# Optimization experiments

Measured on AMD Instinct MI355X. Metric: run time of the kernel, lower is better.

Reference implementation:

```python
import jax, jax.numpy as jnp
import numpy as np

N_HEADS = 12
C = 3          # per-head in/hidden/out channels (12/4)
C_PRED = 1     # predictor hidden (4/4)
BN_EPS = 1e-5
COS_EPS = 1e-8
B, H, W = 8, 512, 768


def setup_inputs() -> dict:
    key = jax.random.key(0)
    ks = jax.random.split(key, 22)
    p = lambda k, s: jax.random.normal(k, s, jnp.float32) * 0.1
    return {
        "latent1": jax.random.normal(ks[0], (B, N_HEADS, H, W), jnp.float32),
        "latent2": jax.random.normal(ks[1], (B, N_HEADS, H, W), jnp.float32),
        # projector conv1 + BN
        "W1": p(ks[2], (N_HEADS, C, C)), "b1": p(ks[3], (N_HEADS, C)),
        "g1": 1.0 + p(ks[4], (N_HEADS, C)), "be1": p(ks[5], (N_HEADS, C)),
        # projector conv2 + BN
        "W2": p(ks[6], (N_HEADS, C, C)), "b2": p(ks[7], (N_HEADS, C)),
        "g2": 1.0 + p(ks[8], (N_HEADS, C)), "be2": p(ks[9], (N_HEADS, C)),
        # projector conv3 + BN (no ReLU)
        "W3": p(ks[10], (N_HEADS, C, C)), "b3": p(ks[11], (N_HEADS, C)),
        "g3": 1.0 + p(ks[12], (N_HEADS, C)), "be3": p(ks[13], (N_HEADS, C)),
        # predictor conv1 + BN
        "W4": p(ks[14], (N_HEADS, C_PRED, C)), "b4": p(ks[15], (N_HEADS, C_PRED)),
        "g4": 1.0 + p(ks[16], (N_HEADS, C_PRED)), "be4": p(ks[17], (N_HEADS, C_PRED)),
        # predictor conv2 (no BN)
        "W5": p(ks[18], (N_HEADS, C, C_PRED)), "b5": p(ks[19], (N_HEADS, C)),
    }


def _conv1x1(x, Wk, bk):
    # x: [B, Cin, H, W'], Wk: [Cout, Cin]
    return jnp.einsum('oc,bchw->bohw', Wk, x) + bk[None, :, None, None]


def _bn(x, g, be):
    # training-mode BatchNorm2d: batch statistics over (B, H, W)
    m = x.mean(axis=(0, 2, 3), keepdims=True)
    v = x.var(axis=(0, 2, 3), keepdims=True)  # biased var, as torch BN uses
    return (x - m) * jax.lax.rsqrt(v + BN_EPS) * g[None, :, None, None] + be[None, :, None, None]


def _cos_loss(p, z):
    # -mean(cosine_similarity(p, detach(z), dim=1))
    z = jax.lax.stop_gradient(z)
    dot = jnp.sum(p * z, axis=1)
    npn = jnp.maximum(jnp.sqrt(jnp.sum(p * p, axis=1)), COS_EPS)
    nzn = jnp.maximum(jnp.sqrt(jnp.sum(z * z, axis=1)), COS_EPS)
    return -jnp.mean(dot / (npn * nzn))


def _head_loss(x1, x2, W1, b1, g1, be1, W2, b2, g2, be2, W3, b3, g3, be3,
               W4, b4, g4, be4, W5, b5):
    def proj(x):
        x = jax.nn.relu(_bn(_conv1x1(x, W1, b1), g1, be1))
        x = jax.nn.relu(_bn(_conv1x1(x, W2, b2), g2, be2))
        return _bn(_conv1x1(x, W3, b3), g3, be3)

    def pred(z):
        h = jax.nn.relu(_bn(_conv1x1(z, W4, b4), g4, be4))
        return _conv1x1(h, W5, b5)

    z1, z2 = proj(x1), proj(x2)
    p1, p2 = pred(z1), pred(z2)
    return 0.5 * (_cos_loss(p1, z2) + _cos_loss(p2, z1))


def reference(latent1, latent2, W1, b1, g1, be1, W2, b2, g2, be2,
              W3, b3, g3, be3, W4, b4, g4, be4, W5, b5):
    Bd, Cd, Hd, Wd = latent1.shape
    Wp = Wd // C
    # per-channel view [B, H, W] -> [B, 3, H, W/3]; stack heads on leading axis
    x1 = latent1.reshape(Bd, N_HEADS, C, Hd, Wp).transpose(1, 0, 2, 3, 4)
    x2 = latent2.reshape(Bd, N_HEADS, C, Hd, Wp).transpose(1, 0, 2, 3, 4)
    losses = jax.vmap(_head_loss)(x1, x2, W1, b1, g1, be1, W2, b2, g2, be2,
                                  W3, b3, g3, be3, W4, b4, g4, be4, W5, b5)
    return jnp.sum(losses)
```

## Files before the change

kernel.cpp:

```cpp
#include <hip/hip_runtime.h>
#include <hip/hip_fp16.h>
#include <math.h>


typedef unsigned short ushort_t;
typedef unsigned int   uint_t;

constexpr int   NH      = 12;
constexpr int   POS     = 131072;
constexpr int   NB      = 8;
constexpr long long MLL = (long long)NB * POS;
constexpr int   CSPAN   = POS / 16;
constexpr int   SBLK    = 128;
constexpr int   NTOT    = NB * NH * 3 * POS;

constexpr size_t P_CNT      = (size_t)24 * SBLK * 9;
constexpr size_t NEED_BYTES = (size_t)NTOT * 2 * 2 + 3 * P_CNT * 8 + 64;

template <int K>
__device__ inline void block_reduce_to0(double (&v)[K]) {
#pragma unroll
  for (int off = 32; off > 0; off >>= 1) {
#pragma unroll
    for (int k = 0; k < K; ++k) v[k] += __shfl_down(v[k], off, 64);
  }
  __shared__ double lds[4][K];
  __syncthreads();
  const int lane = threadIdx.x & 63;
  const int wv   = threadIdx.x >> 6;
  if (lane == 0) {
#pragma unroll
    for (int k = 0; k < K; ++k) lds[wv][k] = v[k];
  }
  __syncthreads();
  if (threadIdx.x == 0) {
#pragma unroll
    for (int k = 0; k < K; ++k) v[k] = lds[0][k] + lds[1][k] + lds[2][k] + lds[3][k];
  }
}

__device__ inline uint_t pack2h(float lo, float hi) {
  return (uint_t)__half_as_ushort(__float2half(lo)) |
         ((uint_t)__half_as_ushort(__float2half(hi)) << 16);
}
__device__ inline float h_lo(uint_t w) {
  return __half2float(__ushort_as_half((unsigned short)(w & 0xFFFFu)));
}
__device__ inline float h_hi(uint_t w) {
  return __half2float(__ushort_as_half((unsigned short)(w >> 16)));
}

template <bool H16>
__device__ inline void load3x8(const float* __restrict__ X,
                               const ushort_t* __restrict__ XH,
                               size_t e, float (&f)[3][8]) {
#pragma unroll
  for (int c = 0; c < 3; ++c) {
    const size_t a = e + (size_t)c * POS;
    if constexpr (H16) {
      const uint4 v = *(const uint4*)(XH + a);
      f[c][0] = h_lo(v.x); f[c][1] = h_hi(v.x);
      f[c][2] = h_lo(v.y); f[c][3] = h_hi(v.y);
      f[c][4] = h_lo(v.z); f[c][5] = h_hi(v.z);
      f[c][6] = h_lo(v.w); f[c][7] = h_hi(v.w);
    } else {
      const float4 u0 = *(const float4*)(X + a);
      const float4 u1 = *(const float4*)(X + a + 4);
      f[c][0] = u0.x; f[c][1] = u0.y; f[c][2] = u0.z; f[c][3] = u0.w;
      f[c][4] = u1.x; f[c][5] = u1.y; f[c][6] = u1.z; f[c][7] = u1.w;
    }
  }
}

__device__ inline void store8h(ushort_t* __restrict__ XH, size_t e,
                               const float (&g)[8]) {
  uint4 h;
  h.x = pack2h(g[0], g[1]);
  h.y = pack2h(g[2], g[3]);
  h.z = pack2h(g[4], g[5]);
  h.w = pack2h(g[6], g[7]);
  *(uint4*)(XH + e) = h;
}

__device__ inline void moments_to_mc(const double (&v)[9], double (&m)[3],
                                     double (&C)[3][3]) {
  const double M = (double)MLL;
  m[0] = v[0] / M; m[1] = v[1] / M; m[2] = v[2] / M;
  C[0][0] = v[3] / M - m[0] * m[0];
  C[1][1] = v[4] / M - m[1] * m[1];
  C[2][2] = v[5] / M - m[2] * m[2];
  C[0][1] = C[1][0] = v[6] / M - m[0] * m[1];
  C[0][2] = C[2][0] = v[7] / M - m[0] * m[2];
  C[1][2] = C[2][1] = v[8] / M - m[1] * m[2];
}

__device__ inline void slice_reduce9(const double* __restrict__ P, int s,
                                     double (&v)[9]) {
#pragma unroll
  for (int k = 0; k < 9; ++k) v[k] = 0.0;
  if (threadIdx.x < SBLK) {
    const double* p = P + ((size_t)s * SBLK + threadIdx.x) * 9;
#pragma unroll
    for (int k = 0; k < 9; ++k) v[k] = p[k];
  }
  block_reduce_to0<9>(v);
}

__device__ inline void fold_math(const double (&v)[9], const float* __restrict__ Wk,
                                 const float* __restrict__ bk,
                                 const float* __restrict__ gk,
                                 const float* __restrict__ bek, int n,
                                 float* __restrict__ dst) {
  double m[3], C[3][3];
  moments_to_mc(v, m, C);
  for (int o = 0; o < 3; ++o) {
    const double w0 = Wk[n * 9 + o * 3 + 0];
    const double w1 = Wk[n * 9 + o * 3 + 1];
    const double w2 = Wk[n * 9 + o * 3 + 2];
    const double my = w0 * m[0] + w1 * m[1] + w2 * m[2] + (double)bk[n * 3 + o];
    const double vy = w0 * w0 * C[0][0] + w1 * w1 * C[1][1] + w2 * w2 * C[2][2] +
                      2.0 * (w0 * w1 * C[0][1] + w0 * w2 * C[0][2] + w1 * w2 * C[1][2]);
    const double sc = (double)gk[n * 3 + o] / sqrt(vy + 1e-5);
    const double tt = (double)bek[n * 3 + o] - my * sc;
    dst[o * 3 + 0] = (float)(sc * w0);
    dst[o * 3 + 1] = (float)(sc * w1);
    dst[o * 3 + 2] = (float)(sc * w2);
    dst[9 + o]     = (float)(sc * (double)bk[n * 3 + o] + tt);
  }
}

__device__ inline void fold34_math(const double (&v)[9], const float* __restrict__ W3,
                                   const float* __restrict__ b3,
                                   const float* __restrict__ g3,
                                   const float* __restrict__ be3,
                                   const float* __restrict__ W4,
                                   const float* __restrict__ b4,
                                   const float* __restrict__ g4,
                                   const float* __restrict__ be4, int n,
                                   float* __restrict__ dst) {
  double m[3], C[3][3];
  moments_to_mc(v, m, C);
  double F3d[3][3], c3d[3];
  for (int o = 0; o < 3; ++o) {
    const double w0 = W3[n * 9 + o * 3 + 0];
    const double w1 = W3[n * 9 + o * 3 + 1];
    const double w2 = W3[n * 9 + o * 3 + 2];
    const double m3 = w0 * m[0] + w1 * m[1] + w2 * m[2] + (double)b3[n * 3 + o];
    const double vy = w0 * w0 * C[0][0] + w1 * w1 * C[1][1] + w2 * w2 * C[2][2] +
                      2.0 * (w0 * w1 * C[0][1] + w0 * w2 * C[0][2] + w1 * w2 * C[1][2]);
    const double s3 = (double)g3[n * 3 + o] / sqrt(vy + 1e-5);
    const double t3 = (double)be3[n * 3 + o] - m3 * s3;
    F3d[o][0] = s3 * w0; F3d[o][1] = s3 * w1; F3d[o][2] = s3 * w2;
    c3d[o] = s3 * (double)b3[n * 3 + o] + t3;
    dst[o * 3 + 0] = (float)F3d[o][0];
    dst[o * 3 + 1] = (float)F3d[o][1];
    dst[o * 3 + 2] = (float)F3d[o][2];
    dst[9 + o]     = (float)c3d[o];
  }
  double q[3] = {0.0, 0.0, 0.0};
  double d = (double)b4[n];
  for (int o = 0; o < 3; ++o) {
    const double w4o = W4[n * 3 + o];
    q[0] += w4o * F3d[o][0];
    q[1] += w4o * F3d[o][1];
    q[2] += w4o * F3d[o][2];
    d += w4o * c3d[o];
  }
  const double m4 = q[0] * m[0] + q[1] * m[1] + q[2] * m[2] + d;
  double v4 = 0.0;
  for (int i = 0; i < 3; ++i)
    for (int j = 0; j < 3; ++j) v4 += q[i] * q[j] * C[i][j];
  const double s4 = (double)g4[n] / sqrt(v4 + 1e-5);
  const double t4 = (double)be4[n] - m4 * s4;
  for (int o = 0; o < 3; ++o) dst[12 + o] = (float)(s4 * (double)W4[n * 3 + o]);
  dst[15] = (float)(s4 * (double)b4[n] + t4);
}

template <bool STORE>
__global__ __launch_bounds__(256) void pass1_kernel(
    const float* __restrict__ x1, const float* __restrict__ x2,
    ushort_t* __restrict__ xh1, ushort_t* __restrict__ xh2,
    double* __restrict__ P0, double* __restrict__ lossAcc,
    uint_t* __restrict__ cnt) {
  if (blockIdx.x == 0 && blockIdx.y == 0 && threadIdx.x == 0) {
    *lossAcc = 0.0;
    *cnt = 0u;
  }
  const int u = blockIdx.y;
  const int s = u % 24;
  const int b = u / 24;
  const int n = s >> 1;
  const float* __restrict__ X = (s & 1) ? x2 : x1;
  ushort_t* __restrict__ XH = (s & 1) ? xh2 : xh1;
  const size_t off0 = (size_t)((b * NH + n) * 3) * POS + (size_t)blockIdx.x * CSPAN;

  float acc[9] = {0.f, 0.f, 0.f, 0.f, 0.f, 0.f, 0.f, 0.f, 0.f};
#pragma unroll 2
  for (int i = 0; i < 4; ++i) {
    const size_t e = off0 + i * 2048 + threadIdx.x * 8;
    float f[3][8];
    load3x8<false>(X, nullptr, e, f);
    if constexpr (STORE) {
#pragma unroll
      for (int c = 0; c < 3; ++c) store8h(XH, e + (size_t)c * POS, f[c]);
    }
#pragma unroll
    for (int j = 0; j < 8; ++j) {
      const float X0 = f[0][j], X1 = f[1][j], X2 = f[2][j];
      acc[0] += X0;      acc[1] += X1;      acc[2] += X2;
      acc[3] += X0 * X0; acc[4] += X1 * X1; acc[5] += X2 * X2;
      acc[6] += X0 * X1; acc[7] += X0 * X2; acc[8] += X1 * X2;
    }
  }
  double v9[9];
#pragma unroll
  for (int k = 0; k < 9; ++k) v9[k] = (double)acc[k];
  block_reduce_to0<9>(v9);
  if (threadIdx.x == 0) {
    double* dst = P0 + ((size_t)s * SBLK + b * 16 + blockIdx.x) * 9;
#pragma unroll
    for (int k = 0; k < 9; ++k) dst[k] = v9[k];
  }
}

template <bool H16>
__global__ __launch_bounds__(256) void pass2_kernel(
    const float* __restrict__ x1, const float* __restrict__ x2,
    const ushort_t* __restrict__ xh1, const ushort_t* __restrict__ xh2,
    const float* __restrict__ W1, const float* __restrict__ b1,
    const float* __restrict__ g1, const float* __restrict__ be1,
    const double* __restrict__ P0, double* __restrict__ P1) {
  const int u = blockIdx.y;
  const int s = u % 24;
  const int b = u / 24;
  const int n = s >> 1;
  const float* __restrict__ X = (s & 1) ? x2 : x1;
  const ushort_t* __restrict__ XH = (s & 1) ? xh2 : xh1;
  const size_t off0 = (size_t)((b * NH + n) * 3) * POS + (size_t)blockIdx.x * CSPAN;

  __shared__ float sf1[12];
  {
    double v[9];
    slice_reduce9(P0, s, v);
    if (threadIdx.x == 0) fold_math(v, W1, b1, g1, be1, n, sf1);
    __syncthreads();
  }
  float w1f[3][3], c1v[3];
#pragma unroll
  for (int o = 0; o < 3; ++o) {
#pragma unroll
    for (int c = 0; c < 3; ++c) w1f[o][c] = sf1[o * 3 + c];
    c1v[o] = sf1[9 + o];
  }

  float acc[9] = {0.f, 0.f, 0.f, 0.f, 0.f, 0.f, 0.f, 0.f, 0.f};
#pragma unroll 2
  for (int i = 0; i < 4; ++i) {
    const size_t e = off0 + i * 2048 + threadIdx.x * 8;
    float f[3][8];
    load3x8<H16>(X, XH, e, f);
#pragma unroll
    for (int j = 0; j < 8; ++j) {
      const float X0 = f[0][j], X1 = f[1][j], X2 = f[2][j];
      const float A0 = fmaxf(0.f, fmaf(w1f[0][0], X0, fmaf(w1f[0][1], X1, fmaf(w1f[0][2], X2, c1v[0]))));
      const float A1 = fmaxf(0.f, fmaf(w1f[1][0], X0, fmaf(w1f[1][1], X1, fmaf(w1f[1][2], X2, c1v[1]))));
      const float A2v= fmaxf(0.f, fmaf(w1f[2][0], X0, fmaf(w1f[2][1], X1, fmaf(w1f[2][2], X2, c1v[2]))));
      acc[0] += A0;       acc[1] += A1;       acc[2] += A2v;
      acc[3] += A0 * A0;  acc[4] += A1 * A1;  acc[5] += A2v * A2v;
      acc[6] += A0 * A1;  acc[7] += A0 * A2v; acc[8] += A1 * A2v;
    }
  }
  double v9[9];
#pragma unroll
  for (int k = 0; k < 9; ++k) v9[k] = (double)acc[k];
  block_reduce_to0<9>(v9);
  if (threadIdx.x == 0) {
    double* dst = P1 + ((size_t)s * SBLK + b * 16 + blockIdx.x) * 9;
#pragma unroll
    for (int k = 0; k < 9; ++k) dst[k] = v9[k];
  }
}

template <bool H16>
__global__ __launch_bounds__(256) void pass3_kernel(
    const float* __restrict__ x1, const float* __restrict__ x2,
    const ushort_t* __restrict__ xh1, const ushort_t* __restrict__ xh2,
    const float* __restrict__ W1, const float* __restrict__ b1,
    const float* __restrict__ g1, const float* __restrict__ be1,
    const float* __restrict__ W2, const float* __restrict__ b2,
    const float* __restrict__ g2, const float* __restrict__ be2,
    const double* __restrict__ P0, const double* __restrict__ P1,
    double* __restrict__ P2) {
  const int u = blockIdx.y;
  const int s = u % 24;
  const int b = u / 24;
  const int n = s >> 1;
  const float* __restrict__ X = (s & 1) ? x2 : x1;
  const ushort_t* __restrict__ XH = (s & 1) ? xh2 : xh1;
  const size_t off0 = (size_t)((b * NH + n) * 3) * POS + (size_t)blockIdx.x * CSPAN;

  __shared__ float sf1[12], sf2[12];
  {
    double v[9];
    slice_reduce9(P0, s, v);
    if (threadIdx.x == 0) fold_math(v, W1, b1, g1, be1, n, sf1);
    slice_reduce9(P1, s, v);
    if (threadIdx.x == 0) fold_math(v, W2, b2, g2, be2, n, sf2);
    __syncthreads();
  }
  float w1f[3][3], c1v[3], w2f[3][3], c2v[3];
#pragma unroll
  for (int o = 0; o < 3; ++o) {
#pragma unroll
    for (int c = 0; c < 3; ++c) {
      w1f[o][c] = sf1[o * 3 + c];
      w2f[o][c] = sf2[o * 3 + c];
    }
    c1v[o] = sf1[9 + o];
    c2v[o] = sf2[9 + o];
  }

  float acc[9] = {0.f, 0.f, 0.f, 0.f, 0.f, 0.f, 0.f, 0.f, 0.f};
#pragma unroll 2
  for (int i = 0; i < 4; ++i) {
    const size_t e = off0 + i * 2048 + threadIdx.x * 8;
    float f[3][8];
    load3x8<H16>(X, XH, e, f);
#pragma unroll
    for (int j = 0; j < 8; ++j) {
      const float X0 = f[0][j], X1 = f[1][j], X2 = f[2][j];
      const float a0 = fmaxf(0.f, fmaf(w1f[0][0], X0, fmaf(w1f[0][1], X1, fmaf(w1f[0][2], X2, c1v[0]))));
      const float a1 = fmaxf(0.f, fmaf(w1f[1][0], X0, fmaf(w1f[1][1], X1, fmaf(w1f[1][2], X2, c1v[1]))));
      const float a2 = fmaxf(0.f, fmaf(w1f[2][0], X0, fmaf(w1f[2][1], X1, fmaf(w1f[2][2], X2, c1v[2]))));
      const float A0 = fmaxf(0.f, fmaf(w2f[0][0], a0, fmaf(w2f[0][1], a1, fmaf(w2f[0][2], a2, c2v[0]))));
      const float A1 = fmaxf(0.f, fmaf(w2f[1][0], a0, fmaf(w2f[1][1], a1, fmaf(w2f[1][2], a2, c2v[1]))));
      const float A2v= fmaxf(0.f, fmaf(w2f[2][0], a0, fmaf(w2f[2][1], a1, fmaf(w2f[2][2], a2, c2v[2]))));
      acc[0] += A0;       acc[1] += A1;       acc[2] += A2v;
      acc[3] += A0 * A0;  acc[4] += A1 * A1;  acc[5] += A2v * A2v;
      acc[6] += A0 * A1;  acc[7] += A0 * A2v; acc[8] += A1 * A2v;
    }
  }
  double v9[9];
#pragma unroll
  for (int k = 0; k < 9; ++k) v9[k] = (double)acc[k];
  block_reduce_to0<9>(v9);
  if (threadIdx.x == 0) {
    double* dst = P2 + ((size_t)s * SBLK + b * 16 + blockIdx.x) * 9;
#pragma unroll
    for (int k = 0; k < 9; ++k) dst[k] = v9[k];
  }
}

__device__ inline void full_chain(const float (&S)[40], const float (&w5)[3],
                                  const float (&b5v)[3], float v0, float v1,
                                  float v2, float (&z)[3], float (&p)[3]) {
  const float t0 = fmaxf(0.f, fmaf(S[0], v0, fmaf(S[1], v1, fmaf(S[2], v2, S[9]))));
  const float t1 = fmaxf(0.f, fmaf(S[3], v0, fmaf(S[4], v1, fmaf(S[5], v2, S[10]))));
  const float t2 = fmaxf(0.f, fmaf(S[6], v0, fmaf(S[7], v1, fmaf(S[8], v2, S[11]))));
  const float a0 = fmaxf(0.f, fmaf(S[12], t0, fmaf(S[13], t1, fmaf(S[14], t2, S[21]))));
  const float a1 = fmaxf(0.f, fmaf(S[15], t0, fmaf(S[16], t1, fmaf(S[17], t2, S[22]))));
  const float a2 = fmaxf(0.f, fmaf(S[18], t0, fmaf(S[19], t1, fmaf(S[20], t2, S[23]))));
  z[0] = fmaf(S[24], a0, fmaf(S[25], a1, fmaf(S[26], a2, S[33])));
  z[1] = fmaf(S[27], a0, fmaf(S[28], a1, fmaf(S[29], a2, S[34])));
  z[2] = fmaf(S[30], a0, fmaf(S[31], a1, fmaf(S[32], a2, S[35])));
  const float y4 = fmaf(S[36], z[0], fmaf(S[37], z[1], fmaf(S[38], z[2], S[39])));
  const float h = fmaxf(0.f, y4);
#pragma unroll
  for (int o = 0; o < 3; ++o) p[o] = fmaf(w5[o], h, b5v[o]);
}

template <bool H16>
__global__ __launch_bounds__(256) void pass4_kernel(
    const float* __restrict__ x1, const float* __restrict__ x2,
    const ushort_t* __restrict__ xh1, const ushort_t* __restrict__ xh2,
    const float* __restrict__ W1, const float* __restrict__ b1,
    const float* __restrict__ g1, const float* __restrict__ be1,
    const float* __restrict__ W2, const float* __restrict__ b2,
    const float* __restrict__ g2, const float* __restrict__ be2,
    const float* __restrict__ W3, const float* __restrict__ b3,
    const float* __restrict__ g3, const float* __restrict__ be3,
    const float* __restrict__ W4, const float* __restrict__ b4,
    const float* __restrict__ g4, const float* __restrict__ be4,
    const float* __restrict__ W5, const float* __restrict__ b5,
    const double* __restrict__ P0, const double* __restrict__ P1,
    const double* __restrict__ P2, double* __restrict__ lossAcc,
    uint_t* __restrict__ cnt, float* __restrict__ out) {
  const int u = blockIdx.y;
  const int n = u % 12;
  const int b = u / 12;
  const size_t off0 = (size_t)((b * NH + n) * 3) * POS + (size_t)blockIdx.x * CSPAN;

  __shared__ float sh[2][40];
  {
    double v[9];
#pragma unroll
    for (int br = 0; br < 2; ++br) {
      const int s = 2 * n + br;
      slice_reduce9(P0, s, v);
      if (threadIdx.x == 0) fold_math(v, W1, b1, g1, be1, n, &sh[br][0]);
      slice_reduce9(P1, s, v);
      if (threadIdx.x == 0) fold_math(v, W2, b2, g2, be2, n, &sh[br][12]);
      slice_reduce9(P2, s, v);
      if (threadIdx.x == 0)
        fold34_math(v, W3, b3, g3, be3, W4, b4, g4, be4, n, &sh[br][24]);
    }
    __syncthreads();
  }
  float S0[40], S1[40];
#pragma unroll
  for (int k = 0; k < 40; ++k) {
    S0[k] = sh[0][k];
    S1[k] = sh[1][k];
  }
  float w5[3], b5v[3];
#pragma unroll
  for (int o = 0; o < 3; ++o) {
    w5[o]  = W5[n * 3 + o];
    b5v[o] = b5[n * 3 + o];
  }

  float acc = 0.f;
  for (int i = 0; i < 4; ++i) {
    const size_t e = off0 + i * 2048 + threadIdx.x * 8;
    float fA[3][8], fB[3][8];
    load3x8<H16>(x1, xh1, e, fA);
    load3x8<H16>(x2, xh2, e, fB);
#pragma unroll
    for (int j = 0; j < 8; ++j) {
      float z1[3], p1[3], z2[3], p2[3];
      full_chain(S0, w5, b5v, fA[0][j], fA[1][j], fA[2][j], z1, p1);
      full_chain(S1, w5, b5v, fB[0][j], fB[1][j], fB[2][j], z2, p2);

      const float d12 = p1[0] * z2[0] + p1[1] * z2[1] + p1[2] * z2[2];
      const float pp1 = p1[0] * p1[0] + p1[1] * p1[1] + p1[2] * p1[2];
      const float zz2 = z2[0] * z2[0] + z2[1] * z2[1] + z2[2] * z2[2];
      acc += d12 * __builtin_amdgcn_rsqf(fmaxf(pp1, 1e-16f)) *
                   __builtin_amdgcn_rsqf(fmaxf(zz2, 1e-16f));

      const float d21 = p2[0] * z1[0] + p2[1] * z1[1] + p2[2] * z1[2];
      const float pp2 = p2[0] * p2[0] + p2[1] * p2[1] + p2[2] * p2[2];
      const float zz1 = z1[0] * z1[0] + z1[1] * z1[1] + z1[2] * z1[2];
      acc += d21 * __builtin_amdgcn_rsqf(fmaxf(pp2, 1e-16f)) *
                   __builtin_amdgcn_rsqf(fmaxf(zz1, 1e-16f));
    }
  }

  double v[1] = {(double)acc};
  block_reduce_to0<1>(v);
  if (threadIdx.x == 0) {
    atomicAdd(lossAcc, v[0]);
    __threadfence();
    const uint_t total = gridDim.x * gridDim.y;
    const uint_t old = atomicAdd(cnt, 1u);
    if (old == total - 1u) {
      __threadfence();
      const double tot = atomicAdd(lossAcc, 0.0);
      out[0] = (float)(-0.5 * tot / (double)MLL);
    }
  }
}

extern "C" void kernel_launch(void* const* d_in, const int* in_sizes, int n_in,
                              void* d_out, int out_size, void* d_ws, size_t ws_size,
                              hipStream_t stream) {
  const float* x1  = (const float*)d_in[0];
  const float* x2  = (const float*)d_in[1];
  const float* W1  = (const float*)d_in[2];
  const float* b1  = (const float*)d_in[3];
  const float* g1  = (const float*)d_in[4];
  const float* be1 = (const float*)d_in[5];
  const float* W2  = (const float*)d_in[6];
  const float* b2  = (const float*)d_in[7];
  const float* g2  = (const float*)d_in[8];
  const float* be2 = (const float*)d_in[9];
  const float* W3  = (const float*)d_in[10];
  const float* b3  = (const float*)d_in[11];
  const float* g3  = (const float*)d_in[12];
  const float* be3 = (const float*)d_in[13];
  const float* W4  = (const float*)d_in[14];
  const float* b4  = (const float*)d_in[15];
  const float* g4  = (const float*)d_in[16];
  const float* be4 = (const float*)d_in[17];
  const float* W5  = (const float*)d_in[18];
  const float* b5  = (const float*)d_in[19];

  const bool big = ws_size >= NEED_BYTES;
  ushort_t* xh1 = nullptr;
  ushort_t* xh2 = nullptr;
  double* dbase;
  if (big) {
    xh1 = (ushort_t*)d_ws;
    xh2 = xh1 + NTOT;
    dbase = (double*)(xh2 + NTOT);
  } else {
    dbase = (double*)d_ws;
  }
  double* P0 = dbase;
  double* P1 = P0 + P_CNT;
  double* P2 = P1 + P_CNT;
  double* lossAcc = P2 + P_CNT;
  uint_t* cnt = (uint_t*)(lossAcc + 1);

  const dim3 blk(256);
  const dim3 gA(16, 192);
  const dim3 gD(16, 96);

  if (big) {
    pass1_kernel<true><<<gA, blk, 0, stream>>>(x1, x2, xh1, xh2, P0, lossAcc, cnt);
    pass2_kernel<true><<<gA, blk, 0, stream>>>(x1, x2, xh1, xh2, W1, b1, g1, be1,
                                               P0, P1);
    pass3_kernel<true><<<gA, blk, 0, stream>>>(x1, x2, xh1, xh2, W1, b1, g1, be1,
                                               W2, b2, g2, be2, P0, P1, P2);
    pass4_kernel<true><<<gD, blk, 0, stream>>>(x1, x2, xh1, xh2, W1, b1, g1, be1,
                                               W2, b2, g2, be2, W3, b3, g3, be3,
                                               W4, b4, g4, be4, W5, b5, P0, P1,
                                               P2, lossAcc, cnt, (float*)d_out);
  } else {
    pass1_kernel<false><<<gA, blk, 0, stream>>>(x1, x2, nullptr, nullptr, P0,
                                                lossAcc, cnt);
    pass2_kernel<false><<<gA, blk, 0, stream>>>(x1, x2, nullptr, nullptr, W1, b1,
                                                g1, be1, P0, P1);
    pass3_kernel<false><<<gA, blk, 0, stream>>>(x1, x2, nullptr, nullptr, W1, b1,
                                                g1, be1, W2, b2, g2, be2, P0, P1,
                                                P2);
    pass4_kernel<false><<<gD, blk, 0, stream>>>(x1, x2, nullptr, nullptr, W1, b1,
                                                g1, be1, W2, b2, g2, be2, W3, b3,
                                                g3, be3, W4, b4, g4, be4, W5, b5,
                                                P0, P1, P2, lossAcc, cnt,
                                                (float*)d_out);
  }
}
```

Before: 580.4 us.

## Hoist BN stat folding into tiny kernels and software-prefetch pass loads

Before, every block of passes 2-4 re-reduced all per-slice partial moments and recomputed the folded BN affine parameters in its prologue. That work now runs once per slice in small stats/fold kernels that write a derived-parameter buffer, and the big passes just read it. The pass loops also explicitly double-buffer the next iteration's vector loads to overlap memory latency with compute. The cost is three extra kernel launches and higher register pressure from the prefetch buffers.

```diff
diff --git a/kernel.cpp b/kernel.cpp
--- a/kernel.cpp
+++ b/kernel.cpp
@@ -15,7 +15,8 @@
 constexpr int   NTOT    = NB * NH * 3 * POS;
 
 constexpr size_t P_CNT      = (size_t)24 * SBLK * 9;
-constexpr size_t NEED_BYTES = (size_t)NTOT * 2 * 2 + 3 * P_CNT * 8 + 64;
+constexpr size_t NEED_BYTES = (size_t)NTOT * 2 * 2 + 3 * P_CNT * 8 + 32 +
+                              (size_t)24 * 40 * 4;
 
 template <int K>
 __device__ inline void block_reduce_to0(double (&v)[K]) {
@@ -43,33 +44,11 @@
   return (uint_t)__half_as_ushort(__float2half(lo)) |
          ((uint_t)__half_as_ushort(__float2half(hi)) << 16);
 }
-__device__ inline float h_lo(uint_t w) {
-  return __half2float(__ushort_as_half((unsigned short)(w & 0xFFFFu)));
-}
-__device__ inline float h_hi(uint_t w) {
-  return __half2float(__ushort_as_half((unsigned short)(w >> 16)));
-}
-
-template <bool H16>
-__device__ inline void load3x8(const float* __restrict__ X,
-                               const ushort_t* __restrict__ XH,
-                               size_t e, float (&f)[3][8]) {
-#pragma unroll
-  for (int c = 0; c < 3; ++c) {
-    const size_t a = e + (size_t)c * POS;
-    if constexpr (H16) {
-      const uint4 v = *(const uint4*)(XH + a);
-      f[c][0] = h_lo(v.x); f[c][1] = h_hi(v.x);
-      f[c][2] = h_lo(v.y); f[c][3] = h_hi(v.y);
-      f[c][4] = h_lo(v.z); f[c][5] = h_hi(v.z);
-      f[c][6] = h_lo(v.w); f[c][7] = h_hi(v.w);
-    } else {
-      const float4 u0 = *(const float4*)(X + a);
-      const float4 u1 = *(const float4*)(X + a + 4);
-      f[c][0] = u0.x; f[c][1] = u0.y; f[c][2] = u0.z; f[c][3] = u0.w;
-      f[c][4] = u1.x; f[c][5] = u1.y; f[c][6] = u1.z; f[c][7] = u1.w;
-    }
-  }
+
+__device__ inline float hget(const uint4& v, int j) {
+  const uint_t w = (&v.x)[j >> 1];
+  return __half2float(__ushort_as_half(
+      (j & 1) ? (unsigned short)(w >> 16) : (unsigned short)(w & 0xFFFFu)));
 }
 
 __device__ inline void store8h(ushort_t* __restrict__ XH, size_t e,
@@ -92,18 +71,6 @@
   C[0][1] = C[1][0] = v[6] / M - m[0] * m[1];
   C[0][2] = C[2][0] = v[7] / M - m[0] * m[2];
   C[1][2] = C[2][1] = v[8] / M - m[1] * m[2];
-}
-
-__device__ inline void slice_reduce9(const double* __restrict__ P, int s,
-                                     double (&v)[9]) {
-#pragma unroll
-  for (int k = 0; k < 9; ++k) v[k] = 0.0;
-  if (threadIdx.x < SBLK) {
-    const double* p = P + ((size_t)s * SBLK + threadIdx.x) * 9;
-#pragma unroll
-    for (int k = 0; k < 9; ++k) v[k] = p[k];
-  }
-  block_reduce_to0<9>(v);
 }
 
 __device__ inline void fold_math(const double (&v)[9], const float* __restrict__ Wk,
@@ -176,6 +143,24 @@
   dst[15] = (float)(s4 * (double)b4[n] + t4);
 }
 
+__device__ inline void acc9(float X0, float X1, float X2, float (&a)[9]) {
+  a[0] += X0;      a[1] += X1;      a[2] += X2;
+  a[3] += X0 * X0; a[4] += X1 * X1; a[5] += X2 * X2;
+  a[6] += X0 * X1; a[7] += X0 * X2; a[8] += X1 * X2;
+}
+
+__device__ inline void load3x8_f32(const float* __restrict__ X, size_t e,
+                                   float (&f)[3][8]) {
+#pragma unroll
+  for (int c = 0; c < 3; ++c) {
+    const size_t a = e + (size_t)c * POS;
+    const float4 u0 = *(const float4*)(X + a);
+    const float4 u1 = *(const float4*)(X + a + 4);
+    f[c][0] = u0.x; f[c][1] = u0.y; f[c][2] = u0.z; f[c][3] = u0.w;
+    f[c][4] = u1.x; f[c][5] = u1.y; f[c][6] = u1.z; f[c][7] = u1.w;
+  }
+}
+
 template <bool STORE>
 __global__ __launch_bounds__(256) void pass1_kernel(
     const float* __restrict__ x1, const float* __restrict__ x2,
@@ -192,26 +177,50 @@
   const int n = s >> 1;
   const float* __restrict__ X = (s & 1) ? x2 : x1;
   ushort_t* __restrict__ XH = (s & 1) ? xh2 : xh1;
+  const int tid = threadIdx.x;
   const size_t off0 = (size_t)((b * NH + n) * 3) * POS + (size_t)blockIdx.x * CSPAN;
 
   float acc[9] = {0.f, 0.f, 0.f, 0.f, 0.f, 0.f, 0.f, 0.f, 0.f};
-#pragma unroll 2
+
+  float4 cur[6];
+#pragma unroll
+  for (int c = 0; c < 3; ++c) {
+    const size_t a = off0 + (size_t)c * POS + tid * 8;
+    cur[2 * c]     = *(const float4*)(X + a);
+    cur[2 * c + 1] = *(const float4*)(X + a + 4);
+  }
+#pragma unroll
   for (int i = 0; i < 4; ++i) {
-    const size_t e = off0 + i * 2048 + threadIdx.x * 8;
+    float4 nxt[6];
+    if (i < 3) {
+#pragma unroll
+      for (int c = 0; c < 3; ++c) {
+        const size_t a = off0 + (size_t)c * POS + (i + 1) * 2048 + tid * 8;
+        nxt[2 * c]     = *(const float4*)(X + a);
+        nxt[2 * c + 1] = *(const float4*)(X + a + 4);
+      }
+    }
+    const size_t e = off0 + i * 2048 + tid * 8;
     float f[3][8];
-    load3x8<false>(X, nullptr, e, f);
+#pragma unroll
+    for (int c = 0; c < 3; ++c) {
+      f[c][0] = cur[2 * c].x;     f[c][1] = cur[2 * c].y;
+      f[c][2] = cur[2 * c].z;     f[c][3] = cur[2 * c].w;
+      f[c][4] = cur[2 * c + 1].x; f[c][5] = cur[2 * c + 1].y;
+      f[c][6] = cur[2 * c + 1].z; f[c][7] = cur[2 * c + 1].w;
+    }
     if constexpr (STORE) {
 #pragma unroll
       for (int c = 0; c < 3; ++c) store8h(XH, e + (size_t)c * POS, f[c]);
     }
 #pragma unroll
-    for (int j = 0; j < 8; ++j) {
-      const float X0 = f[0][j], X1 = f[1][j], X2 = f[2][j];
-      acc[0] += X0;      acc[1] += X1;      acc[2] += X2;
-      acc[3] += X0 * X0; acc[4] += X1 * X1; acc[5] += X2 * X2;
-      acc[6] += X0 * X1; acc[7] += X0 * X2; acc[8] += X1 * X2;
-    }
-  }
+    for (int j = 0; j < 8; ++j) acc9(f[0][j], f[1][j], f[2][j], acc);
+    if (i < 3) {
+#pragma unroll
+      for (int k = 0; k < 6; ++k) cur[k] = nxt[k];
+    }
+  }
+
   double v9[9];
 #pragma unroll
   for (int k = 0; k < 9; ++k) v9[k] = (double)acc[k];
@@ -223,53 +232,109 @@
   }
 }
 
+__global__ __launch_bounds__(256) void stats_fold_kernel(
+    const double* __restrict__ P, const float* __restrict__ Wk,
+    const float* __restrict__ bk, const float* __restrict__ gk,
+    const float* __restrict__ bek, float* __restrict__ derived, int outoff) {
+  const int s = blockIdx.x;
+  double v[9] = {0, 0, 0, 0, 0, 0, 0, 0, 0};
+  if (threadIdx.x < SBLK) {
+    const double* p = P + ((size_t)s * SBLK + threadIdx.x) * 9;
+#pragma unroll
+    for (int k = 0; k < 9; ++k) v[k] = p[k];
+  }
+  block_reduce_to0<9>(v);
+  if (threadIdx.x == 0)
+    fold_math(v, Wk, bk, gk, bek, s >> 1, derived + s * 40 + outoff);
+}
+
+__global__ __launch_bounds__(256) void stats34_kernel(
+    const double* __restrict__ P2, const float* __restrict__ W3,
+    const float* __restrict__ b3, const float* __restrict__ g3,
+    const float* __restrict__ be3, const float* __restrict__ W4,
+    const float* __restrict__ b4, const float* __restrict__ g4,
+    const float* __restrict__ be4, float* __restrict__ derived) {
+  const int s = blockIdx.x;
+  double v[9] = {0, 0, 0, 0, 0, 0, 0, 0, 0};
+  if (threadIdx.x < SBLK) {
+    const double* p = P2 + ((size_t)s * SBLK + threadIdx.x) * 9;
+#pragma unroll
+    for (int k = 0; k < 9; ++k) v[k] = p[k];
+  }
+  block_reduce_to0<9>(v);
+  if (threadIdx.x == 0)
+    fold34_math(v, W3, b3, g3, be3, W4, b4, g4, be4, s >> 1,
+                derived + s * 40 + 24);
+}
+
 template <bool H16>
 __global__ __launch_bounds__(256) void pass2_kernel(
     const float* __restrict__ x1, const float* __restrict__ x2,
     const ushort_t* __restrict__ xh1, const ushort_t* __restrict__ xh2,
-    const float* __restrict__ W1, const float* __restrict__ b1,
-    const float* __restrict__ g1, const float* __restrict__ be1,
-    const double* __restrict__ P0, double* __restrict__ P1) {
+    const float* __restrict__ derived, double* __restrict__ P1) {
   const int u = blockIdx.y;
   const int s = u % 24;
   const int b = u / 24;
   const int n = s >> 1;
   const float* __restrict__ X = (s & 1) ? x2 : x1;
   const ushort_t* __restrict__ XH = (s & 1) ? xh2 : xh1;
+  const int tid = threadIdx.x;
   const size_t off0 = (size_t)((b * NH + n) * 3) * POS + (size_t)blockIdx.x * CSPAN;
 
-  __shared__ float sf1[12];
-  {
-    double v[9];
-    slice_reduce9(P0, s, v);
-    if (threadIdx.x == 0) fold_math(v, W1, b1, g1, be1, n, sf1);
-    __syncthreads();
-  }
+  const float* D = derived + s * 40;
   float w1f[3][3], c1v[3];
 #pragma unroll
   for (int o = 0; o < 3; ++o) {
 #pragma unroll
-    for (int c = 0; c < 3; ++c) w1f[o][c] = sf1[o * 3 + c];
-    c1v[o] = sf1[9 + o];
+    for (int c = 0; c < 3; ++c) w1f[o][c] = D[o * 3 + c];
+    c1v[o] = D[9 + o];
   }
 
   float acc[9] = {0.f, 0.f, 0.f, 0.f, 0.f, 0.f, 0.f, 0.f, 0.f};
-#pragma unroll 2
-  for (int i = 0; i < 4; ++i) {
-    const size_t e = off0 + i * 2048 + threadIdx.x * 8;
-    float f[3][8];
-    load3x8<H16>(X, XH, e, f);
-#pragma unroll
-    for (int j = 0; j < 8; ++j) {
-      const float X0 = f[0][j], X1 = f[1][j], X2 = f[2][j];
-      const float A0 = fmaxf(0.f, fmaf(w1f[0][0], X0, fmaf(w1f[0][1], X1, fmaf(w1f[0][2], X2, c1v[0]))));
-      const float A1 = fmaxf(0.f, fmaf(w1f[1][0], X0, fmaf(w1f[1][1], X1, fmaf(w1f[1][2], X2, c1v[1]))));
-      const float A2v= fmaxf(0.f, fmaf(w1f[2][0], X0, fmaf(w1f[2][1], X1, fmaf(w1f[2][2], X2, c1v[2]))));
-      acc[0] += A0;       acc[1] += A1;       acc[2] += A2v;
-      acc[3] += A0 * A0;  acc[4] += A1 * A1;  acc[5] += A2v * A2v;
-      acc[6] += A0 * A1;  acc[7] += A0 * A2v; acc[8] += A1 * A2v;
-    }
-  }
+
+  if constexpr (H16) {
+    uint4 cur[3];
+#pragma unroll
+    for (int c = 0; c < 3; ++c)
+      cur[c] = *(const uint4*)(XH + off0 + (size_t)c * POS + tid * 8);
+#pragma unroll
+    for (int i = 0; i < 4; ++i) {
+      uint4 nxt[3];
+      if (i < 3) {
+#pragma unroll
+        for (int c = 0; c < 3; ++c)
+          nxt[c] = *(const uint4*)(XH + off0 + (size_t)c * POS + (i + 1) * 2048 +
+                                   tid * 8);
+      }
+#pragma unroll
+      for (int j = 0; j < 8; ++j) {
+        const float X0 = hget(cur[0], j), X1 = hget(cur[1], j), X2 = hget(cur[2], j);
+        const float A0 = fmaxf(0.f, fmaf(w1f[0][0], X0, fmaf(w1f[0][1], X1, fmaf(w1f[0][2], X2, c1v[0]))));
+        const float A1 = fmaxf(0.f, fmaf(w1f[1][0], X0, fmaf(w1f[1][1], X1, fmaf(w1f[1][2], X2, c1v[1]))));
+        const float A2 = fmaxf(0.f, fmaf(w1f[2][0], X0, fmaf(w1f[2][1], X1, fmaf(w1f[2][2], X2, c1v[2]))));
+        acc9(A0, A1, A2, acc);
+      }
+      if (i < 3) {
+#pragma unroll
+        for (int c = 0; c < 3; ++c) cur[c] = nxt[c];
+      }
+    }
+  } else {
+    for (int i = 0; i < 4; ++i) {
+      const size_t e = off0 + i * 2048 + tid * 8;
+      float f[3][8];
+      load3x8_f32(X, e, f);
+#pragma unroll
+      for (int j = 0; j < 8; ++j) {
+        const float X0 = f[0][j], X1 = f[1][j], X2 = f[2][j];
+        const float A0 = fmaxf(0.f, fmaf(w1f[0][0], X0, fmaf(w1f[0][1], X1, fmaf(w1f[0][2], X2, c1v[0]))));
+        const float A1 = fmaxf(0.f, fmaf(w1f[1][0], X0, fmaf(w1f[1][1], X1, fmaf(w1f[1][2], X2, c1v[1]))));
+        const float A2 = fmaxf(0.f, fmaf(w1f[2][0], X0, fmaf(w1f[2][1], X1, fmaf(w1f[2][2], X2, c1v[2]))));
+        acc9(A0, A1, A2, acc);
+      }
+    }
+  }
+
   double v9[9];
 #pragma unroll
   for (int k = 0; k < 9; ++k) v9[k] = (double)acc[k];
@@ -285,61 +350,73 @@
 __global__ __launch_bounds__(256) void pass3_kernel(
     const float* __restrict__ x1, const float* __restrict__ x2,
     const ushort_t* __restrict__ xh1, const ushort_t* __restrict__ xh2,
-    const float* __restrict__ W1, const float* __restrict__ b1,
-    const float* __restrict__ g1, const float* __restrict__ be1,
-    const float* __restrict__ W2, const float* __restrict__ b2,
-    const float* __restrict__ g2, const float* __restrict__ be2,
-    const double* __restrict__ P0, const double* __restrict__ P1,
-    double* __restrict__ P2) {
+    const float* __restrict__ derived, double* __restrict__ P2) {
   const int u = blockIdx.y;
   const int s = u % 24;
   const int b = u / 24;
   const int n = s >> 1;
   const float* __restrict__ X = (s & 1) ? x2 : x1;
   const ushort_t* __restrict__ XH = (s & 1) ? xh2 : xh1;
+  const int tid = threadIdx.x;
   const size_t off0 = (size_t)((b * NH + n) * 3) * POS + (size_t)blockIdx.x * CSPAN;
 
-  __shared__ float sf1[12], sf2[12];
-  {
-    double v[9];
-    slice_reduce9(P0, s, v);
-    if (threadIdx.x == 0) fold_math(v, W1, b1, g1, be1, n, sf1);
-    slice_reduce9(P1, s, v);
-    if (threadIdx.x == 0) fold_math(v, W2, b2, g2, be2, n, sf2);
-    __syncthreads();
-  }
+  const float* D = derived + s * 40;
   float w1f[3][3], c1v[3], w2f[3][3], c2v[3];
 #pragma unroll
   for (int o = 0; o < 3; ++o) {
 #pragma unroll
     for (int c = 0; c < 3; ++c) {
-      w1f[o][c] = sf1[o * 3 + c];
-      w2f[o][c] = sf2[o * 3 + c];
-    }
-    c1v[o] = sf1[9 + o];
-    c2v[o] = sf2[9 + o];
+      w1f[o][c] = D[o * 3 + c];
+      w2f[o][c] = D[12 + o * 3 + c];
+    }
+    c1v[o] = D[9 + o];
+    c2v[o] = D[21 + o];
   }
 
   float acc[9] = {0.f, 0.f, 0.f, 0.f, 0.f, 0.f, 0.f, 0.f, 0.f};
-#pragma unroll 2
-  for (int i = 0; i < 4; ++i) {
-    const size_t e = off0 + i * 2048 + threadIdx.x * 8;
-    float f[3][8];
-    load3x8<H16>(X, XH, e, f);
-#pragma unroll
-    for (int j = 0; j < 8; ++j) {
-      const float X0 = f[0][j], X1 = f[1][j], X2 = f[2][j];
-      const float a0 = fmaxf(0.f, fmaf(w1f[0][0], X0, fmaf(w1f[0][1], X1, fmaf(w1f[0][2], X2, c1v[0]))));
-      const float a1 = fmaxf(0.f, fmaf(w1f[1][0], X0, fmaf(w1f[1][1], X1, fmaf(w1f[1][2], X2, c1v[1]))));
-      const float a2 = fmaxf(0.f, fmaf(w1f[2][0], X0, fmaf(w1f[2][1], X1, fmaf(w1f[2][2], X2, c1v[2]))));
-      const float A0 = fmaxf(0.f, fmaf(w2f[0][0], a0, fmaf(w2f[0][1], a1, fmaf(w2f[0][2], a2, c2v[0]))));
-      const float A1 = fmaxf(0.f, fmaf(w2f[1][0], a0, fmaf(w2f[1][1], a1, fmaf(w2f[1][2], a2, c2v[1]))));
-      const float A2v= fmaxf(0.f, fmaf(w2f[2][0], a0, fmaf(w2f[2][1], a1, fmaf(w2f[2][2], a2, c2v[2]))));
-      acc[0] += A0;       acc[1] += A1;       acc[2] += A2v;
-      acc[3] += A0 * A0;  acc[4] += A1 * A1;  acc[5] += A2v * A2v;
-      acc[6] += A0 * A1;  acc[7] += A0 * A2v; acc[8] += A1 * A2v;
-    }
-  }
+
+  auto body = [&](float X0, float X1, float X2) {
+    const float a0 = fmaxf(0.f, fmaf(w1f[0][0], X0, fmaf(w1f[0][1], X1, fmaf(w1f[0][2], X2, c1v[0]))));
+    const float a1 = fmaxf(0.f, fmaf(w1f[1][0], X0, fmaf(w1f[1][1], X1, fmaf(w1f[1][2], X2, c1v[1]))));
+    const float a2 = fmaxf(0.f, fmaf(w1f[2][0], X0, fmaf(w1f[2][1], X1, fmaf(w1f[2][2], X2, c1v[2]))));
+    const float A0 = fmaxf(0.f, fmaf(w2f[0][0], a0, fmaf(w2f[0][1], a1, fmaf(w2f[0][2], a2, c2v[0]))));
+    const float A1 = fmaxf(0.f, fmaf(w2f[1][0], a0, fmaf(w2f[1][1], a1, fmaf(w2f[1][2], a2, c2v[1]))));
+    const float A2 = fmaxf(0.f, fmaf(w2f[2][0], a0, fmaf(w2f[2][1], a1, fmaf(w2f[2][2], a2, c2v[2]))));
+    acc9(A0, A1, A2, acc);
+  };
+
+  if constexpr (H16) {
+    uint4 cur[3];
+#pragma unroll
+    for (int c = 0; c < 3; ++c)
+      cur[c] = *(const uint4*)(XH + off0 + (size_t)c * POS + tid * 8);
+#pragma unroll
+    for (int i = 0; i < 4; ++i) {
+      uint4 nxt[3];
+      if (i < 3) {
+#pragma unroll
+        for (int c = 0; c < 3; ++c)
+          nxt[c] = *(const uint4*)(XH + off0 + (size_t)c * POS + (i + 1) * 2048 +
+                                   tid * 8);
+      }
+#pragma unroll
+      for (int j = 0; j < 8; ++j)
+        body(hget(cur[0], j), hget(cur[1], j), hget(cur[2], j));
+      if (i < 3) {
+#pragma unroll
+        for (int c = 0; c < 3; ++c) cur[c] = nxt[c];
+      }
+    }
+  } else {
+    for (int i = 0; i < 4; ++i) {
+      const size_t e = off0 + i * 2048 + tid * 8;
+      float f[3][8];
+      load3x8_f32(X, e, f);
+#pragma unroll
+      for (int j = 0; j < 8; ++j) body(f[0][j], f[1][j], f[2][j]);
+    }
+  }
+
   double v9[9];
 #pragma unroll
   for (int k = 0; k < 9; ++k) v9[k] = (double)acc[k];
@@ -373,44 +450,24 @@
 __global__ __launch_bounds__(256) void pass4_kernel(
     const float* __restrict__ x1, const float* __restrict__ x2,
     const ushort_t* __restrict__ xh1, const ushort_t* __restrict__ xh2,
-    const float* __restrict__ W1, const float* __restrict__ b1,
-    const float* __restrict__ g1, const float* __restrict__ be1,
-    const float* __restrict__ W2, const float* __restrict__ b2,
-    const float* __restrict__ g2, const float* __restrict__ be2,
-    const float* __restrict__ W3, const float* __restrict__ b3,
-    const float* __restrict__ g3, const float* __restrict__ be3,
-    const float* __restrict__ W4, const float* __restrict__ b4,
-    const float* __restrict__ g4, const float* __restrict__ be4,
     const float* __restrict__ W5, const float* __restrict__ b5,
-    const double* __restrict__ P0, const double* __restrict__ P1,
-    const double* __restrict__ P2, double* __restrict__ lossAcc,
+    const float* __restrict__ derived, double* __restrict__ lossAcc,
     uint_t* __restrict__ cnt, float* __restrict__ out) {
   const int u = blockIdx.y;
   const int n = u % 12;
   const int b = u / 12;
+  const int tid = threadIdx.x;
   const size_t off0 = (size_t)((b * NH + n) * 3) * POS + (size_t)blockIdx.x * CSPAN;
 
-  __shared__ float sh[2][40];
+  float S0[40], S1[40];
   {
-    double v[9];
-#pragma unroll
-    for (int br = 0; br < 2; ++br) {
-      const int s = 2 * n + br;
-      slice_reduce9(P0, s, v);
-      if (threadIdx.x == 0) fold_math(v, W1, b1, g1, be1, n, &sh[br][0]);
-      slice_reduce9(P1, s, v);
-      if (threadIdx.x == 0) fold_math(v, W2, b2, g2, be2, n, &sh[br][12]);
-      slice_reduce9(P2, s, v);
-      if (threadIdx.x == 0)
-        fold34_math(v, W3, b3, g3, be3, W4, b4, g4, be4, n, &sh[br][24]);
-    }
-    __syncthreads();
-  }
-  float S0[40], S1[40];
-#pragma unroll
-  for (int k = 0; k < 40; ++k) {
-    S0[k] = sh[0][k];
-    S1[k] = sh[1][k];
+    const float* D0 = derived + (size_t)(2 * n + 0) * 40;
+    const float* D1 = derived + (size_t)(2 * n + 1) * 40;
+#pragma unroll
+    for (int k = 0; k < 40; ++k) {
+      S0[k] = D0[k];
+      S1[k] = D1[k];
+    }
   }
   float w5[3], b5v[3];
 #pragma unroll
@@ -420,28 +477,64 @@
   }
 
   float acc = 0.f;
-  for (int i = 0; i < 4; ++i) {
-    const size_t e = off0 + i * 2048 + threadIdx.x * 8;
-    float fA[3][8], fB[3][8];
-    load3x8<H16>(x1, xh1, e, fA);
-    load3x8<H16>(x2, xh2, e, fB);
-#pragma unroll
-    for (int j = 0; j < 8; ++j) {
-      float z1[3], p1[3], z2[3], p2[3];
-      full_chain(S0, w5, b5v, fA[0][j], fA[1][j], fA[2][j], z1, p1);
-      full_chain(S1, w5, b5v, fB[0][j], fB[1][j], fB[2][j], z2, p2);
-
-      const float d12 = p1[0] * z2[0] + p1[1] * z2[1] + p1[2] * z2[2];
-      const float pp1 = p1[0] * p1[0] + p1[1] * p1[1] + p1[2] * p1[2];
-      const float zz2 = z2[0] * z2[0] + z2[1] * z2[1] + z2[2] * z2[2];
-      acc += d12 * __builtin_amdgcn_rsqf(fmaxf(pp1, 1e-16f)) *
-                   __builtin_amdgcn_rsqf(fmaxf(zz2, 1e-16f));
-
-      const float d21 = p2[0] * z1[0] + p2[1] * z1[1] + p2[2] * z1[2];
-      const float pp2 = p2[0] * p2[0] + p2[1] * p2[1] + p2[2] * p2[2];
-      const float zz1 = z1[0] * z1[0] + z1[1] * z1[1] + z1[2] * z1[2];
-      acc += d21 * __builtin_amdgcn_rsqf(fmaxf(pp2, 1e-16f)) *
-                   __builtin_amdgcn_rsqf(fmaxf(zz1, 1e-16f));
+
+  auto body = [&](float xA0, float xA1, float xA2, float xB0, float xB1,
+                  float xB2) {
+    float z1[3], p1[3], z2[3], p2[3];
+    full_chain(S0, w5, b5v, xA0, xA1, xA2, z1, p1);
+    full_chain(S1, w5, b5v, xB0, xB1, xB2, z2, p2);
+    const float d12 = p1[0] * z2[0] + p1[1] * z2[1] + p1[2] * z2[2];
+    const float pp1 = p1[0] * p1[0] + p1[1] * p1[1] + p1[2] * p1[2];
+    const float zz2 = z2[0] * z2[0] + z2[1] * z2[1] + z2[2] * z2[2];
+    acc += d12 * __builtin_amdgcn_rsqf(fmaxf(pp1, 1e-16f)) *
+                 __builtin_amdgcn_rsqf(fmaxf(zz2, 1e-16f));
+    const float d21 = p2[0] * z1[0] + p2[1] * z1[1] + p2[2] * z1[2];
+    const float pp2 = p2[0] * p2[0] + p2[1] * p2[1] + p2[2] * p2[2];
+    const float zz1 = z1[0] * z1[0] + z1[1] * z1[1] + z1[2] * z1[2];
+    acc += d21 * __builtin_amdgcn_rsqf(fmaxf(pp2, 1e-16f)) *
+                 __builtin_amdgcn_rsqf(fmaxf(zz1, 1e-16f));
+  };
+
+  if constexpr (H16) {
+    uint4 curA[3], curB[3];
+#pragma unroll
+    for (int c = 0; c < 3; ++c) {
+      const size_t a = off0 + (size_t)c * POS + tid * 8;
+      curA[c] = *(const uint4*)(xh1 + a);
+      curB[c] = *(const uint4*)(xh2 + a);
+    }
+#pragma unroll
+    for (int i = 0; i < 4; ++i) {
+      uint4 nxtA[3], nxtB[3];
+      if (i < 3) {
+#pragma unroll
+        for (int c = 0; c < 3; ++c) {
+          const size_t a = off0 + (size_t)c * POS + (i + 1) * 2048 + tid * 8;
+          nxtA[c] = *(const uint4*)(xh1 + a);
+          nxtB[c] = *(const uint4*)(xh2 + a);
+        }
+      }
+#pragma unroll
+      for (int j = 0; j < 8; ++j)
+        body(hget(curA[0], j), hget(curA[1], j), hget(curA[2], j),
+             hget(curB[0], j), hget(curB[1], j), hget(curB[2], j));
+      if (i < 3) {
+#pragma unroll
+        for (int c = 0; c < 3; ++c) {
+          curA[c] = nxtA[c];
+          curB[c] = nxtB[c];
+        }
+      }
+    }
+  } else {
+    for (int i = 0; i < 4; ++i) {
+      const size_t e = off0 + i * 2048 + tid * 8;
+      float fA[3][8], fB[3][8];
+      load3x8_f32(x1, e, fA);
+      load3x8_f32(x2, e, fB);
+#pragma unroll
+      for (int j = 0; j < 8; ++j)
+        body(fA[0][j], fA[1][j], fA[2][j], fB[0][j], fB[1][j], fB[2][j]);
     }
   }
 
@@ -500,6 +593,7 @@
   double* P2 = P1 + P_CNT;
   double* lossAcc = P2 + P_CNT;
   uint_t* cnt = (uint_t*)(lossAcc + 1);
+  float* derived = (float*)(lossAcc + 2);
 
   const dim3 blk(256);
   const dim3 gA(16, 192);
@@ -507,26 +601,27 @@
 
   if (big) {
     pass1_kernel<true><<<gA, blk, 0, stream>>>(x1, x2, xh1, xh2, P0, lossAcc, cnt);
-    pass2_kernel<true><<<gA, blk, 0, stream>>>(x1, x2, xh1, xh2, W1, b1, g1, be1,
-                                               P0, P1);
-    pass3_kernel<true><<<gA, blk, 0, stream>>>(x1, x2, xh1, xh2, W1, b1, g1, be1,
-                                               W2, b2, g2, be2, P0, P1, P2);
-    pass4_kernel<true><<<gD, blk, 0, stream>>>(x1, x2, xh1, xh2, W1, b1, g1, be1,
-                                               W2, b2, g2, be2, W3, b3, g3, be3,
-                                               W4, b4, g4, be4, W5, b5, P0, P1,
-                                               P2, lossAcc, cnt, (float*)d_out);
+    stats_fold_kernel<<<24, blk, 0, stream>>>(P0, W1, b1, g1, be1, derived, 0);
+    pass2_kernel<true><<<gA, blk, 0, stream>>>(x1, x2, xh1, xh2, derived, P1);
+    stats_fold_kernel<<<24, blk, 0, stream>>>(P1, W2, b2, g2, be2, derived, 12);
+    pass3_kernel<true><<<gA, blk, 0, stream>>>(x1, x2, xh1, xh2, derived, P2);
+    stats34_kernel<<<24, blk, 0, stream>>>(P2, W3, b3, g3, be3, W4, b4, g4, be4,
+                                           derived);
+    pass4_kernel<true><<<gD, blk, 0, stream>>>(x1, x2, xh1, xh2, W5, b5, derived,
+                                               lossAcc, cnt, (float*)d_out);
   } else {
     pass1_kernel<false><<<gA, blk, 0, stream>>>(x1, x2, nullptr, nullptr, P0,
                                                 lossAcc, cnt);
-    pass2_kernel<false><<<gA, blk, 0, stream>>>(x1, x2, nullptr, nullptr, W1, b1,
-                                                g1, be1, P0, P1);
-    pass3_kernel<false><<<gA, blk, 0, stream>>>(x1, x2, nullptr, nullptr, W1, b1,
-                                                g1, be1, W2, b2, g2, be2, P0, P1,
+    stats_fold_kernel<<<24, blk, 0, stream>>>(P0, W1, b1, g1, be1, derived, 0);
+    pass2_kernel<false><<<gA, blk, 0, stream>>>(x1, x2, nullptr, nullptr, derived,
+                                                P1);
+    stats_fold_kernel<<<24, blk, 0, stream>>>(P1, W2, b2, g2, be2, derived, 12);
+    pass3_kernel<false><<<gA, blk, 0, stream>>>(x1, x2, nullptr, nullptr, derived,
                                                 P2);
-    pass4_kernel<false><<<gD, blk, 0, stream>>>(x1, x2, nullptr, nullptr, W1, b1,
-                                                g1, be1, W2, b2, g2, be2, W3, b3,
-                                                g3, be3, W4, b4, g4, be4, W5, b5,
-                                                P0, P1, P2, lossAcc, cnt,
+    stats34_kernel<<<24, blk, 0, stream>>>(P2, W3, b3, g3, be3, W4, b4, g4, be4,
+                                           derived);
+    pass4_kernel<false><<<gD, blk, 0, stream>>>(x1, x2, nullptr, nullptr, W5, b5,
+                                                derived, lossAcc, cnt,
                                                 (float*)d_out);
   }
 }
```

After: 499.1 us. 1.16x faster.
